# Optimization experiments

Hardware: AMD Instinct MI355X
Metric: run time of the kernel (lower is better)

The kernel has to match this reference:

```python
import jax, jax.numpy as jnp
import numpy as np

N = 50000      # nodes
E = 800000     # edges (before self-loops)
H = 4          # heads
NEG_SLOPE = 0.2
EPS = 1e-16


def setup_inputs() -> dict:
    key = jax.random.key(0)
    ks = jax.random.split(key, 10)
    m, hidden, m_y = 128, 32, 32
    x = jax.random.normal(ks[0], (N, m), jnp.float32)
    edge_index = jax.random.randint(ks[1], (2, E), 0, N, jnp.int32)
    s1 = 1.0 / np.sqrt(m)
    s2 = 1.0 / np.sqrt(H * hidden)
    W1 = jax.random.normal(ks[2], (m, H * hidden), jnp.float32) * s1
    a1_src = jax.random.normal(ks[3], (H, hidden), jnp.float32) * s1
    a1_dst = jax.random.normal(ks[4], (H, hidden), jnp.float32) * s1
    b1 = jnp.zeros((H * hidden,), jnp.float32)
    W2 = jax.random.normal(ks[5], (H * hidden, H * m_y), jnp.float32) * s2
    a2_src = jax.random.normal(ks[6], (H, m_y), jnp.float32) * s2
    a2_dst = jax.random.normal(ks[7], (H, m_y), jnp.float32) * s2
    b2 = jnp.zeros((H * m_y,), jnp.float32)
    return {"x": x, "edge_index": edge_index, "W1": W1, "a1_src": a1_src,
            "a1_dst": a1_dst, "b1": b1, "W2": W2, "a2_src": a2_src,
            "a2_dst": a2_dst, "b2": b2}


def gat_conv(x, W, a_src, a_dst, bias, src, dst):
    # x: [N, F_in], W: [F_in, H*C]
    C = a_src.shape[1]
    h = (x @ W).reshape(N, H, C)                      # [N, H, C]
    alpha_s = jnp.einsum('nhc,hc->nh', h, a_src)       # [N, H]
    alpha_d = jnp.einsum('nhc,hc->nh', h, a_dst)       # [N, H]
    e = jax.nn.leaky_relu(alpha_s[src] + alpha_d[dst], NEG_SLOPE)  # [Etot, H]
    # segment softmax over incoming edges of each dst node
    e_max = jax.ops.segment_max(e, dst, num_segments=N)            # [N, H]
    e_exp = jnp.exp(e - e_max[dst])
    denom = jax.ops.segment_sum(e_exp, dst, num_segments=N)        # [N, H]
    alpha = e_exp / (denom[dst] + EPS)                             # [Etot, H]
    out = jax.ops.segment_sum(h[src] * alpha[:, :, None], dst, num_segments=N)
    return out.reshape(N, H * C) + bias


def reference(x, edge_index, W1, a1_src, a1_dst, b1, W2, a2_src, a2_dst, b2):
    # add self-loops (PyG GATConv default add_self_loops=True)
    loops = jnp.arange(N, dtype=edge_index.dtype)
    src = jnp.concatenate([edge_index[0], loops])
    dst = jnp.concatenate([edge_index[1], loops])
    out = gat_conv(x, W1, a1_src, a1_dst, b1, src, dst)
    out = jax.nn.elu(out)
    # dropout(p=0.8) is identity in eval mode
    out = gat_conv(out, W2, a2_src, a2_dst, b2, src, dst)
    return out
```

## Files before the change

kernel.cpp:

```cpp
#include <hip/hip_runtime.h>
#include <math.h>
#include <stdint.h>

typedef __attribute__((ext_vector_type(8))) short short8;
typedef __attribute__((ext_vector_type(4))) float f32x4;

static __device__ __forceinline__ float lrelu(float x) { return x >= 0.f ? x : 0.2f * x; }

static __device__ __forceinline__ uint32_t f2bf(float f) {
    uint32_t u = __float_as_uint(f);
    return (u + 0x7FFFu + ((u >> 16) & 1u)) >> 16;
}

__global__ __launch_bounds__(256) void count_wprep(const int* __restrict__ dst, int E, int N,
                                                   int* __restrict__ deg8,
                                                   int* __restrict__ rank, int eb,
                                                   const float* __restrict__ W1,
                                                   const float* __restrict__ W2,
                                                   uint16_t* __restrict__ wtb1,
                                                   uint16_t* __restrict__ wtb2) {
    if ((int)blockIdx.x < eb) {
        int i = blockIdx.x * 256 + threadIdx.x;
        int p = blockIdx.x & 7;
        if (i < E) rank[i] = atomicAdd(&deg8[p * N + dst[i]], 1);
    } else {
        int idx = (blockIdx.x - eb) * 256 + threadIdx.x;
        const float* src = (idx < 16384) ? W1 : W2;
        uint16_t* dw = (idx < 16384) ? wtb1 : wtb2;
        int j = idx & 16383;
        dw[(j & 127) * 128 + (j >> 7)] = (uint16_t)f2bf(src[j]);
    }
}

__global__ __launch_bounds__(256) void scan1(const int* __restrict__ deg8, int N, int ntot,
                                             int* __restrict__ deg,
                                             int* __restrict__ base8,
                                             int* __restrict__ rowptr,
                                             int* __restrict__ csum) {
    __shared__ int s[256];
    int t = threadIdx.x;
    int i = blockIdx.x * 256 + t;
    int v = 0;
    if (i < N) {
        int total = 0;
        #pragma unroll
        for (int p = 0; p < 8; ++p) {
            int c = deg8[p * N + i];
            base8[p * N + i] = total;
            total += c;
        }
        deg[i] = total;
        v = (total + 15) & ~15;
    }
    s[t] = v;
    __syncthreads();
    #pragma unroll
    for (int off = 1; off < 256; off <<= 1) {
        int add = (t >= off) ? s[t - off] : 0;
        __syncthreads();
        s[t] += add;
        __syncthreads();
    }
    if (i < ntot) rowptr[i] = s[t] - v;
    if (t == 255) csum[blockIdx.x] = s[255];
}

__global__ __launch_bounds__(256) void scan2(const int* __restrict__ csum,
                                             int* __restrict__ coff, int nch) {
    __shared__ int s[256];
    int t = threadIdx.x;
    int v = (t < nch) ? csum[t] : 0;
    s[t] = v;
    __syncthreads();
    #pragma unroll
    for (int off = 1; off < 256; off <<= 1) {
        int add = (t >= off) ? s[t - off] : 0;
        __syncthreads();
        s[t] += add;
        __syncthreads();
    }
    coff[t] = s[t] - v;
}

__global__ __launch_bounds__(256) void scan3(int* __restrict__ rowptr,
                                             const int* __restrict__ coff, int ntot) {
    int i = blockIdx.x * 256 + threadIdx.x;
    if (i < ntot) rowptr[i] += coff[blockIdx.x];
}

__global__ __launch_bounds__(256) void fill_pad(const int* __restrict__ src,
                                                const int* __restrict__ dst,
                                                const int* __restrict__ rank, int E, int N,
                                                const int* __restrict__ rowptr,
                                                const int* __restrict__ deg,
                                                const int* __restrict__ base8,
                                                uint16_t* __restrict__ colidx,
                                                float* __restrict__ as_,
                                                uint32_t* __restrict__ hbf, int eb) {
    if ((int)blockIdx.x < eb) {
        int i = blockIdx.x * 256 + threadIdx.x;
        int p = blockIdx.x & 7;
        if (i < E) {
            int d = dst[i];
            colidx[rowptr[d] + base8[p * N + d] + rank[i]] = (uint16_t)src[i];
        }
    } else {
        int i = (blockIdx.x - eb) * 256 + threadIdx.x;
        if (i < 4) as_[N * 4 + i] = -1e30f;
        if (i < 64) hbf[(size_t)N * 64 + i] = 0u;
        if (i < N) {
            int b = rowptr[i] + deg[i];
            int e = rowptr[i + 1];
            for (int pp = b; pp < e; ++pp) colidx[pp] = (uint16_t)N;
        }
    }
}

__global__ __launch_bounds__(256) void gemm_mfma(const float* __restrict__ x,
                                                 const uint16_t* __restrict__ wtb,
                                                 const float* __restrict__ a_src,
                                                 const float* __restrict__ a_dst,
                                                 uint32_t* __restrict__ hbf,
                                                 float* __restrict__ as_,
                                                 float* __restrict__ ad_,
                                                 int nrows) {
    __shared__ __align__(16) char lds[52224];
    const int t = threadIdx.x;
    const int row0 = blockIdx.x * 64;

    {
        int r = t >> 2;
        int k16b = (t & 3) * 4;
        const float* xrow = x + (size_t)(row0 + r) * 128;
        bool ok = (row0 + r) < nrows;
        #pragma unroll
        for (int i = 0; i < 4; ++i) {
            int k16 = k16b + i;
            float4 va = make_float4(0.f, 0.f, 0.f, 0.f), vb = va;
            if (ok) {
                va = *(const float4*)(xrow + k16 * 8);
                vb = *(const float4*)(xrow + k16 * 8 + 4);
            }
            uint4 pk;
            pk.x = f2bf(va.x) | (f2bf(va.y) << 16);
            pk.y = f2bf(va.z) | (f2bf(va.w) << 16);
            pk.z = f2bf(vb.x) | (f2bf(vb.y) << 16);
            pk.w = f2bf(vb.z) | (f2bf(vb.w) << 16);
            *(uint4*)(lds + r * 272 + k16 * 16) = pk;
        }
    }
    {
        #pragma unroll
        for (int i = 0; i < 8; ++i) {
            int u = t * 8 + i;
            int col = u >> 4, k16 = u & 15;
            uint4 v = *(const uint4*)(wtb + col * 128 + k16 * 8);
            *(uint4*)(lds + 17408 + col * 272 + k16 * 16) = v;
        }
    }
    __syncthreads();

    const int w = t >> 6, lane = t & 63;
    const int wrow0 = w * 16;
    const int la = lane & 15, lb = lane >> 4;

    f32x4 acc[8];
    #pragma unroll
    for (int ct = 0; ct < 8; ++ct) acc[ct] = (f32x4){0.f, 0.f, 0.f, 0.f};

    const char* xsb = lds + (wrow0 + la) * 272;
    const char* wsb = lds + 17408;
    #pragma unroll
    for (int kc = 0; kc < 4; ++kc) {
        int k16 = kc * 4 + lb;
        short8 a = *(const short8*)(xsb + k16 * 16);
        #pragma unroll
        for (int ct = 0; ct < 8; ++ct) {
            int col = ct * 16 + la;
            short8 b = *(const short8*)(wsb + col * 272 + k16 * 16);
            acc[ct] = __builtin_amdgcn_mfma_f32_16x16x32_bf16(a, b, acc[ct], 0, 0, 0);
        }
    }
    __syncthreads();

    float* scr = (float*)lds;
    #pragma unroll
    for (int ct = 0; ct < 8; ++ct)
        #pragma unroll
        for (int r2 = 0; r2 < 4; ++r2)
            scr[(wrow0 + lb * 4 + r2) * 132 + ct * 16 + la] = acc[ct][r2];
    __syncthreads();

    {
        int row = t >> 2, q = t & 3;
        int grow = row0 + row;
        float v[32];
        #pragma unroll
        for (int m = 0; m < 8; ++m) {
            float4 f = *(const float4*)(scr + row * 132 + q * 32 + m * 4);
            v[m * 4 + 0] = f.x; v[m * 4 + 1] = f.y;
            v[m * 4 + 2] = f.z; v[m * 4 + 3] = f.w;
        }
        if (grow < nrows) {
            uint32_t* orow = hbf + (size_t)grow * 64 + q * 16;
            #pragma unroll
            for (int m2 = 0; m2 < 4; ++m2) {
                uint4 pk;
                pk.x = f2bf(v[m2 * 8 + 0]) | (f2bf(v[m2 * 8 + 1]) << 16);
                pk.y = f2bf(v[m2 * 8 + 2]) | (f2bf(v[m2 * 8 + 3]) << 16);
                pk.z = f2bf(v[m2 * 8 + 4]) | (f2bf(v[m2 * 8 + 5]) << 16);
                pk.w = f2bf(v[m2 * 8 + 6]) | (f2bf(v[m2 * 8 + 7]) << 16);
                *(uint4*)(orow + m2 * 4) = pk;
            }
            float ps = 0.f, pd = 0.f;
            const float* asp = a_src + q * 32;
            const float* adp = a_dst + q * 32;
            #pragma unroll
            for (int j = 0; j < 32; ++j) {
                ps = fmaf(v[j], asp[j], ps);
                pd = fmaf(v[j], adp[j], pd);
            }
            as_[grow * 4 + q] = ps;
            ad_[grow * 4 + q] = pd;
        }
    }
}

__global__ __launch_bounds__(256) void aggregate(const uint32_t* __restrict__ hb,
                                                 const float* __restrict__ as_,
                                                 const float* __restrict__ ad_,
                                                 const int* __restrict__ rowptr,
                                                 const uint16_t* __restrict__ colidx,
                                                 const float* __restrict__ bias,
                                                 float* __restrict__ out, int n, int do_elu) {
    int node = blockIdx.x * 4 + (threadIdx.x >> 6);
    if (node >= n) return;
    int lane = threadIdx.x & 63;
    int hd = lane >> 4;
    int k = lane * 2;
    int ce = lane >> 2;
    int ch = lane & 3;
    float adn = ad_[node * 4 + hd];
    float adc = ad_[node * 4 + ch];
    float accx = 0.f, accy = 0.f, denom = 0.f;

    {
        float wgt = __expf(lrelu(as_[node * 4 + hd] + adn));
        uint32_t u = hb[(size_t)node * 64 + lane];
        accx = fmaf(wgt, __uint_as_float(u << 16), accx);
        accy = fmaf(wgt, __uint_as_float(u & 0xFFFF0000u), accy);
        denom += wgt;
    }
    const int beg = rowptr[node], end = rowptr[node + 1];
    for (int j = beg; j < end; j += 16) {
        uint4 cA = *(const uint4*)(colidx + j);
        uint4 cB = *(const uint4*)(colidx + j + 8);
        int sE[16];
        sE[0]  = cA.x & 0xFFFF; sE[1]  = cA.x >> 16;
        sE[2]  = cA.y & 0xFFFF; sE[3]  = cA.y >> 16;
        sE[4]  = cA.z & 0xFFFF; sE[5]  = cA.z >> 16;
        sE[6]  = cA.w & 0xFFFF; sE[7]  = cA.w >> 16;
        sE[8]  = cB.x & 0xFFFF; sE[9]  = cB.x >> 16;
        sE[10] = cB.y & 0xFFFF; sE[11] = cB.y >> 16;
        sE[12] = cB.z & 0xFFFF; sE[13] = cB.z >> 16;
        sE[14] = cB.w & 0xFFFF; sE[15] = cB.w >> 16;
        int sw = colidx[j + ce];
        float aw = as_[sw * 4 + ch];
        uint32_t u[16];
        #pragma unroll
        for (int e = 0; e < 16; ++e) u[e] = hb[(size_t)sE[e] * 64 + lane];
        float w = __expf(lrelu(aw + adc));
        #pragma unroll
        for (int e = 0; e < 16; ++e) {
            float we = __shfl(w, e * 4 + hd);
            accx = fmaf(we, __uint_as_float(u[e] << 16), accx);
            accy = fmaf(we, __uint_as_float(u[e] & 0xFFFF0000u), accy);
            denom += we;
        }
    }
    float inv = 1.f / (denom + 1e-16f);
    float o0 = fmaf(accx, inv, bias[k]);
    float o1 = fmaf(accy, inv, bias[k + 1]);
    if (do_elu) {
        o0 = o0 > 0.f ? o0 : (__expf(o0) - 1.f);
        o1 = o1 > 0.f ? o1 : (__expf(o1) - 1.f);
    }
    *(float2*)&out[(size_t)node * 128 + k] = make_float2(o0, o1);
}

extern "C" void kernel_launch(void* const* d_in, const int* in_sizes, int n_in,
                              void* d_out, int out_size, void* d_ws, size_t ws_size,
                              hipStream_t stream) {
    const float* x   = (const float*)d_in[0];
    const int*   ei  = (const int*)d_in[1];
    const float* W1  = (const float*)d_in[2];
    const float* a1s = (const float*)d_in[3];
    const float* a1d = (const float*)d_in[4];
    const float* b1  = (const float*)d_in[5];
    const float* W2  = (const float*)d_in[6];
    const float* a2s = (const float*)d_in[7];
    const float* a2d = (const float*)d_in[8];
    const float* b2  = (const float*)d_in[9];
    float* out = (float*)d_out;

    const int N = in_sizes[0] / 128;
    const int E = in_sizes[1] / 2;
    const int* esrc = ei;
    const int* edst = ei + E;

    char* w = (char*)d_ws;
    uint32_t* hbf  = (uint32_t*)w; w += (size_t)(N + 1) * 64 * 4;
    float*    as_  = (float*)w;    w += (size_t)(N + 1) * 4 * 4;
    float*    ad_  = (float*)w;    w += (size_t)(N + 1) * 4 * 4;
    int* deg    = (int*)w;   w += (size_t)N * 4;
    int* rowptr = (int*)w;   w += (size_t)(N + 1) * 4;
    int* rank   = (int*)w;   w += (size_t)E * 4;
    int* deg8   = (int*)w;   w += (size_t)8 * N * 4;
    int* base8  = (int*)w;   w += (size_t)8 * N * 4;
    int* csum   = (int*)w;   w += 256 * 4;
    int* coff   = (int*)w;   w += 256 * 4;
    uint16_t* wtb1 = (uint16_t*)w; w += 16384 * 2;
    uint16_t* wtb2 = (uint16_t*)w; w += 16384 * 2;
    w = (char*)(((uintptr_t)w + 31) & ~(uintptr_t)31);
    uint16_t* colidx = (uint16_t*)w; w += ((size_t)E + 16ull * N) * 2;
    float* out1 = out;

    hipMemsetAsync(deg8, 0, (size_t)8 * N * 4, stream);

    const int eb = (E + 255) / 256;
    const int ntot = N + 1;
    const int nch = (ntot + 255) / 256;
    const int gb = (N + 63) / 64;
    const int nb = (N + 3) / 4;
    const int pb = (N + 255) / 256;

    count_wprep<<<eb + 128, 256, 0, stream>>>(edst, E, N, deg8, rank, eb,
                                              W1, W2, wtb1, wtb2);
    scan1<<<nch, 256, 0, stream>>>(deg8, N, ntot, deg, base8, rowptr, csum);
    scan2<<<1, 256, 0, stream>>>(csum, coff, nch);
    scan3<<<nch, 256, 0, stream>>>(rowptr, coff, ntot);
    fill_pad<<<eb + pb, 256, 0, stream>>>(esrc, edst, rank, E, N, rowptr, deg,
                                          base8, colidx, as_, hbf, eb);

    gemm_mfma<<<gb, 256, 0, stream>>>(x, wtb1, a1s, a1d, hbf, as_, ad_, N);
    aggregate<<<nb, 256, 0, stream>>>(hbf, as_, ad_, rowptr, colidx, b1, out1, N, 1);

    gemm_mfma<<<gb, 256, 0, stream>>>(out1, wtb2, a2s, a2d, hbf, as_, ad_, N);
    aggregate<<<nb, 256, 0, stream>>>(hbf, as_, ad_, rowptr, colidx, b2, out, N, 0);
}
```

Before: 261.7 us.

## Split aggregate wavefront into four edge groups using 16-byte row gathers

Reorganizes the per-node aggregation so each wavefront splits into four 16-lane groups. Each group gathers a full 256-byte bf16 feature row with uint4 loads, and the four groups work on different edges at the same time. Partial sums are combined with cross-group shuffles and the self-loop term is added at the end. This replaces sixteen 4-byte per-lane gathers per chunk with four 16-byte gathers and fewer shuffles, aiming to raise memory-level efficiency. The cost is more accumulator registers, a final reduction, and only a quarter of the lanes doing the store.

New measurement: 265.2 us. Within noise of the previous version (+1.3%).

```diff
diff --git a/kernel.cpp b/kernel.cpp
--- a/kernel.cpp
+++ b/kernel.cpp
@@ -11,6 +11,8 @@
     uint32_t u = __float_as_uint(f);
     return (u + 0x7FFFu + ((u >> 16) & 1u)) >> 16;
 }
+static __device__ __forceinline__ float bflo(uint32_t u) { return __uint_as_float(u << 16); }
+static __device__ __forceinline__ float bfhi(uint32_t u) { return __uint_as_float(u & 0xFFFF0000u); }
 
 __global__ __launch_bounds__(256) void count_wprep(const int* __restrict__ dst, int E, int N,
                                                    int* __restrict__ deg8,
@@ -235,57 +237,94 @@
                                                  float* __restrict__ out, int n, int do_elu) {
     int node = blockIdx.x * 4 + (threadIdx.x >> 6);
     if (node >= n) return;
-    int lane = threadIdx.x & 63;
-    int hd = lane >> 4;
-    int k = lane * 2;
-    int ce = lane >> 2;
-    int ch = lane & 3;
+    int L = threadIdx.x & 63;
+    int g16 = L & 15;
+    int grp = L >> 4;
+    int hd = g16 >> 2;
+    int cw_e = L >> 2;
+    int cw_h = L & 3;
     float adn = ad_[node * 4 + hd];
-    float adc = ad_[node * 4 + ch];
-    float accx = 0.f, accy = 0.f, denom = 0.f;
-
-    {
-        float wgt = __expf(lrelu(as_[node * 4 + hd] + adn));
-        uint32_t u = hb[(size_t)node * 64 + lane];
-        accx = fmaf(wgt, __uint_as_float(u << 16), accx);
-        accy = fmaf(wgt, __uint_as_float(u & 0xFFFF0000u), accy);
-        denom += wgt;
-    }
+    float adc = ad_[node * 4 + cw_h];
+
+    float acc[8];
+    #pragma unroll
+    for (int i = 0; i < 8; ++i) acc[i] = 0.f;
+    float den = 0.f;
+
     const int beg = rowptr[node], end = rowptr[node + 1];
     for (int j = beg; j < end; j += 16) {
-        uint4 cA = *(const uint4*)(colidx + j);
-        uint4 cB = *(const uint4*)(colidx + j + 8);
-        int sE[16];
-        sE[0]  = cA.x & 0xFFFF; sE[1]  = cA.x >> 16;
-        sE[2]  = cA.y & 0xFFFF; sE[3]  = cA.y >> 16;
-        sE[4]  = cA.z & 0xFFFF; sE[5]  = cA.z >> 16;
-        sE[6]  = cA.w & 0xFFFF; sE[7]  = cA.w >> 16;
-        sE[8]  = cB.x & 0xFFFF; sE[9]  = cB.x >> 16;
-        sE[10] = cB.y & 0xFFFF; sE[11] = cB.y >> 16;
-        sE[12] = cB.z & 0xFFFF; sE[13] = cB.z >> 16;
-        sE[14] = cB.w & 0xFFFF; sE[15] = cB.w >> 16;
-        int sw = colidx[j + ce];
-        float aw = as_[sw * 4 + ch];
-        uint32_t u[16];
-        #pragma unroll
-        for (int e = 0; e < 16; ++e) u[e] = hb[(size_t)sE[e] * 64 + lane];
-        float w = __expf(lrelu(aw + adc));
-        #pragma unroll
-        for (int e = 0; e < 16; ++e) {
-            float we = __shfl(w, e * 4 + hd);
-            accx = fmaf(we, __uint_as_float(u[e] << 16), accx);
-            accy = fmaf(we, __uint_as_float(u[e] & 0xFFFF0000u), accy);
-            denom += we;
-        }
-    }
-    float inv = 1.f / (denom + 1e-16f);
-    float o0 = fmaf(accx, inv, bias[k]);
-    float o1 = fmaf(accy, inv, bias[k + 1]);
-    if (do_elu) {
-        o0 = o0 > 0.f ? o0 : (__expf(o0) - 1.f);
-        o1 = o1 > 0.f ? o1 : (__expf(o1) - 1.f);
-    }
-    *(float2*)&out[(size_t)node * 128 + k] = make_float2(o0, o1);
+        int sw = colidx[j + cw_e];
+        float w = __expf(lrelu(as_[sw * 4 + cw_h] + adc));
+        uint4 u0, u1, u2, u3;
+        {
+            int s0 = colidx[j + grp];
+            int s1 = colidx[j + 4 + grp];
+            int s2 = colidx[j + 8 + grp];
+            int s3 = colidx[j + 12 + grp];
+            u0 = *(const uint4*)(hb + (size_t)s0 * 64 + g16 * 4);
+            u1 = *(const uint4*)(hb + (size_t)s1 * 64 + g16 * 4);
+            u2 = *(const uint4*)(hb + (size_t)s2 * 64 + g16 * 4);
+            u3 = *(const uint4*)(hb + (size_t)s3 * 64 + g16 * 4);
+        }
+        float w0 = __shfl(w, ((0 * 4 + grp) << 2) | hd);
+        float w1 = __shfl(w, ((1 * 4 + grp) << 2) | hd);
+        float w2 = __shfl(w, ((2 * 4 + grp) << 2) | hd);
+        float w3 = __shfl(w, ((3 * 4 + grp) << 2) | hd);
+        acc[0] = fmaf(w0, bflo(u0.x), acc[0]); acc[1] = fmaf(w0, bfhi(u0.x), acc[1]);
+        acc[2] = fmaf(w0, bflo(u0.y), acc[2]); acc[3] = fmaf(w0, bfhi(u0.y), acc[3]);
+        acc[4] = fmaf(w0, bflo(u0.z), acc[4]); acc[5] = fmaf(w0, bfhi(u0.z), acc[5]);
+        acc[6] = fmaf(w0, bflo(u0.w), acc[6]); acc[7] = fmaf(w0, bfhi(u0.w), acc[7]);
+        acc[0] = fmaf(w1, bflo(u1.x), acc[0]); acc[1] = fmaf(w1, bfhi(u1.x), acc[1]);
+        acc[2] = fmaf(w1, bflo(u1.y), acc[2]); acc[3] = fmaf(w1, bfhi(u1.y), acc[3]);
+        acc[4] = fmaf(w1, bflo(u1.z), acc[4]); acc[5] = fmaf(w1, bfhi(u1.z), acc[5]);
+        acc[6] = fmaf(w1, bflo(u1.w), acc[6]); acc[7] = fmaf(w1, bfhi(u1.w), acc[7]);
+        acc[0] = fmaf(w2, bflo(u2.x), acc[0]); acc[1] = fmaf(w2, bfhi(u2.x), acc[1]);
+        acc[2] = fmaf(w2, bflo(u2.y), acc[2]); acc[3] = fmaf(w2, bfhi(u2.y), acc[3]);
+        acc[4] = fmaf(w2, bflo(u2.z), acc[4]); acc[5] = fmaf(w2, bfhi(u2.z), acc[5]);
+        acc[6] = fmaf(w2, bflo(u2.w), acc[6]); acc[7] = fmaf(w2, bfhi(u2.w), acc[7]);
+        acc[0] = fmaf(w3, bflo(u3.x), acc[0]); acc[1] = fmaf(w3, bfhi(u3.x), acc[1]);
+        acc[2] = fmaf(w3, bflo(u3.y), acc[2]); acc[3] = fmaf(w3, bfhi(u3.y), acc[3]);
+        acc[4] = fmaf(w3, bflo(u3.z), acc[4]); acc[5] = fmaf(w3, bfhi(u3.z), acc[5]);
+        acc[6] = fmaf(w3, bflo(u3.w), acc[6]); acc[7] = fmaf(w3, bfhi(u3.w), acc[7]);
+        den += (w0 + w1) + (w2 + w3);
+    }
+
+    #pragma unroll
+    for (int i = 0; i < 8; ++i) {
+        acc[i] += __shfl_xor(acc[i], 16);
+        acc[i] += __shfl_xor(acc[i], 32);
+    }
+    den += __shfl_xor(den, 16);
+    den += __shfl_xor(den, 32);
+
+    {
+        float ws = __expf(lrelu(as_[node * 4 + hd] + adn));
+        uint4 us = *(const uint4*)(hb + (size_t)node * 64 + g16 * 4);
+        acc[0] = fmaf(ws, bflo(us.x), acc[0]); acc[1] = fmaf(ws, bfhi(us.x), acc[1]);
+        acc[2] = fmaf(ws, bflo(us.y), acc[2]); acc[3] = fmaf(ws, bfhi(us.y), acc[3]);
+        acc[4] = fmaf(ws, bflo(us.z), acc[4]); acc[5] = fmaf(ws, bfhi(us.z), acc[5]);
+        acc[6] = fmaf(ws, bflo(us.w), acc[6]); acc[7] = fmaf(ws, bfhi(us.w), acc[7]);
+        den += ws;
+    }
+
+    if (grp == 0) {
+        float inv = 1.f / (den + 1e-16f);
+        float4 b0 = *(const float4*)(bias + g16 * 8);
+        float4 b1 = *(const float4*)(bias + g16 * 8 + 4);
+        float o[8];
+        o[0] = fmaf(acc[0], inv, b0.x); o[1] = fmaf(acc[1], inv, b0.y);
+        o[2] = fmaf(acc[2], inv, b0.z); o[3] = fmaf(acc[3], inv, b0.w);
+        o[4] = fmaf(acc[4], inv, b1.x); o[5] = fmaf(acc[5], inv, b1.y);
+        o[6] = fmaf(acc[6], inv, b1.z); o[7] = fmaf(acc[7], inv, b1.w);
+        if (do_elu) {
+            #pragma unroll
+            for (int i = 0; i < 8; ++i)
+                o[i] = o[i] > 0.f ? o[i] : (__expf(o[i]) - 1.f);
+        }
+        float* orow = out + (size_t)node * 128 + g16 * 8;
+        *(float4*)orow       = make_float4(o[0], o[1], o[2], o[3]);
+        *(float4*)(orow + 4) = make_float4(o[4], o[5], o[6], o[7]);
+    }
 }
 
 extern "C" void kernel_launch(void* const* d_in, const int* in_sizes, int n_in,
```

## Split features into eight column slices and aggregate each slice separately

Applied to the files above, without the earlier changes.

The bf16 node-feature table is stored as eight column slices (16 features each, 32 bytes per node) instead of one 256-byte row per node. Aggregation launches 8x the blocks, one per slice, so each slice table is smaller and more likely to stay in cache during random gathers; within a wave, lanes split edges into groups and reduce by shuffle. The self-loop now sits in the padded CSR (one extra slot per row) instead of being a special case. In exchange, attention weights are recomputed eight times per edge and each wave does less useful work per gather.

Result: slower. 484.3 us (+85.1%).

```diff
diff --git a/kernel.cpp b/kernel.cpp
--- a/kernel.cpp
+++ b/kernel.cpp
@@ -11,6 +11,8 @@
     uint32_t u = __float_as_uint(f);
     return (u + 0x7FFFu + ((u >> 16) & 1u)) >> 16;
 }
+static __device__ __forceinline__ float bflo(uint32_t u) { return __uint_as_float(u << 16); }
+static __device__ __forceinline__ float bfhi(uint32_t u) { return __uint_as_float(u & 0xFFFF0000u); }
 
 __global__ __launch_bounds__(256) void count_wprep(const int* __restrict__ dst, int E, int N,
                                                    int* __restrict__ deg8,
@@ -50,7 +52,7 @@
             total += c;
         }
         deg[i] = total;
-        v = (total + 15) & ~15;
+        v = (total + 16) & ~15;
     }
     s[t] = v;
     __syncthreads();
@@ -96,7 +98,8 @@
                                                 const int* __restrict__ base8,
                                                 uint16_t* __restrict__ colidx,
                                                 float* __restrict__ as_,
-                                                uint32_t* __restrict__ hbf, int eb) {
+                                                uint32_t* __restrict__ hbh, int eb) {
+    int N1 = N + 1;
     if ((int)blockIdx.x < eb) {
         int i = blockIdx.x * 256 + threadIdx.x;
         int p = blockIdx.x & 7;
@@ -107,11 +110,12 @@
     } else {
         int i = (blockIdx.x - eb) * 256 + threadIdx.x;
         if (i < 4) as_[N * 4 + i] = -1e30f;
-        if (i < 64) hbf[(size_t)N * 64 + i] = 0u;
+        if (i < 64) hbh[(size_t)(i >> 3) * (N1 * 8) + (size_t)N * 8 + (i & 7)] = 0u;
         if (i < N) {
             int b = rowptr[i] + deg[i];
             int e = rowptr[i + 1];
-            for (int pp = b; pp < e; ++pp) colidx[pp] = (uint16_t)N;
+            colidx[b] = (uint16_t)i;
+            for (int pp = b + 1; pp < e; ++pp) colidx[pp] = (uint16_t)N;
         }
     }
 }
@@ -120,10 +124,10 @@
                                                  const uint16_t* __restrict__ wtb,
                                                  const float* __restrict__ a_src,
                                                  const float* __restrict__ a_dst,
-                                                 uint32_t* __restrict__ hbf,
+                                                 uint32_t* __restrict__ hbh,
                                                  float* __restrict__ as_,
                                                  float* __restrict__ ad_,
-                                                 int nrows) {
+                                                 int nrows, int N1) {
     __shared__ __align__(16) char lds[52224];
     const int t = threadIdx.x;
     const int row0 = blockIdx.x * 64;
@@ -202,16 +206,18 @@
             v[m * 4 + 2] = f.z; v[m * 4 + 3] = f.w;
         }
         if (grow < nrows) {
-            uint32_t* orow = hbf + (size_t)grow * 64 + q * 16;
+            uint4 pk[4];
             #pragma unroll
             for (int m2 = 0; m2 < 4; ++m2) {
-                uint4 pk;
-                pk.x = f2bf(v[m2 * 8 + 0]) | (f2bf(v[m2 * 8 + 1]) << 16);
-                pk.y = f2bf(v[m2 * 8 + 2]) | (f2bf(v[m2 * 8 + 3]) << 16);
-                pk.z = f2bf(v[m2 * 8 + 4]) | (f2bf(v[m2 * 8 + 5]) << 16);
-                pk.w = f2bf(v[m2 * 8 + 6]) | (f2bf(v[m2 * 8 + 7]) << 16);
-                *(uint4*)(orow + m2 * 4) = pk;
+                pk[m2].x = f2bf(v[m2 * 8 + 0]) | (f2bf(v[m2 * 8 + 1]) << 16);
+                pk[m2].y = f2bf(v[m2 * 8 + 2]) | (f2bf(v[m2 * 8 + 3]) << 16);
+                pk[m2].z = f2bf(v[m2 * 8 + 4]) | (f2bf(v[m2 * 8 + 5]) << 16);
+                pk[m2].w = f2bf(v[m2 * 8 + 6]) | (f2bf(v[m2 * 8 + 7]) << 16);
             }
+            uint32_t* r0 = hbh + (size_t)(2 * q) * (N1 * 8) + (size_t)grow * 8;
+            uint32_t* r1 = hbh + (size_t)(2 * q + 1) * (N1 * 8) + (size_t)grow * 8;
+            *(uint4*)r0 = pk[0]; *(uint4*)(r0 + 4) = pk[1];
+            *(uint4*)r1 = pk[2]; *(uint4*)(r1 + 4) = pk[3];
             float ps = 0.f, pd = 0.f;
             const float* asp = a_src + q * 32;
             const float* adp = a_dst + q * 32;
@@ -226,66 +232,53 @@
     }
 }
 
-__global__ __launch_bounds__(256) void aggregate(const uint32_t* __restrict__ hb,
+__global__ __launch_bounds__(256) void aggregate(const uint32_t* __restrict__ hbh,
                                                  const float* __restrict__ as_,
                                                  const float* __restrict__ ad_,
                                                  const int* __restrict__ rowptr,
                                                  const uint16_t* __restrict__ colidx,
                                                  const float* __restrict__ bias,
-                                                 float* __restrict__ out, int n, int do_elu) {
-    int node = blockIdx.x * 4 + (threadIdx.x >> 6);
+                                                 float* __restrict__ out,
+                                                 int n, int N1, int do_elu) {
+    int b = blockIdx.x;
+    int s = b & 7;
+    int node = (b >> 3) * 4 + (threadIdx.x >> 6);
     if (node >= n) return;
-    int lane = threadIdx.x & 63;
-    int hd = lane >> 4;
-    int k = lane * 2;
-    int ce = lane >> 2;
-    int ch = lane & 3;
-    float adn = ad_[node * 4 + hd];
-    float adc = ad_[node * 4 + ch];
-    float accx = 0.f, accy = 0.f, denom = 0.f;
-
-    {
-        float wgt = __expf(lrelu(as_[node * 4 + hd] + adn));
-        uint32_t u = hb[(size_t)node * 64 + lane];
-        accx = fmaf(wgt, __uint_as_float(u << 16), accx);
-        accy = fmaf(wgt, __uint_as_float(u & 0xFFFF0000u), accy);
-        denom += wgt;
-    }
+    int h = s >> 1;
+    int L = threadIdx.x & 63;
+    int d = L & 7;
+    int g = L >> 3;
+    const uint32_t* hb = hbh + (size_t)s * (N1 * 8);
+    float adn = ad_[node * 4 + h];
+    float ax = 0.f, ay = 0.f, den = 0.f;
+
     const int beg = rowptr[node], end = rowptr[node + 1];
     for (int j = beg; j < end; j += 16) {
-        uint4 cA = *(const uint4*)(colidx + j);
-        uint4 cB = *(const uint4*)(colidx + j + 8);
-        int sE[16];
-        sE[0]  = cA.x & 0xFFFF; sE[1]  = cA.x >> 16;
-        sE[2]  = cA.y & 0xFFFF; sE[3]  = cA.y >> 16;
-        sE[4]  = cA.z & 0xFFFF; sE[5]  = cA.z >> 16;
-        sE[6]  = cA.w & 0xFFFF; sE[7]  = cA.w >> 16;
-        sE[8]  = cB.x & 0xFFFF; sE[9]  = cB.x >> 16;
-        sE[10] = cB.y & 0xFFFF; sE[11] = cB.y >> 16;
-        sE[12] = cB.z & 0xFFFF; sE[13] = cB.z >> 16;
-        sE[14] = cB.w & 0xFFFF; sE[15] = cB.w >> 16;
-        int sw = colidx[j + ce];
-        float aw = as_[sw * 4 + ch];
-        uint32_t u[16];
-        #pragma unroll
-        for (int e = 0; e < 16; ++e) u[e] = hb[(size_t)sE[e] * 64 + lane];
-        float w = __expf(lrelu(aw + adc));
-        #pragma unroll
-        for (int e = 0; e < 16; ++e) {
-            float we = __shfl(w, e * 4 + hd);
-            accx = fmaf(we, __uint_as_float(u[e] << 16), accx);
-            accy = fmaf(we, __uint_as_float(u[e] & 0xFFFF0000u), accy);
-            denom += we;
-        }
-    }
-    float inv = 1.f / (denom + 1e-16f);
-    float o0 = fmaf(accx, inv, bias[k]);
-    float o1 = fmaf(accy, inv, bias[k + 1]);
-    if (do_elu) {
-        o0 = o0 > 0.f ? o0 : (__expf(o0) - 1.f);
-        o1 = o1 > 0.f ? o1 : (__expf(o1) - 1.f);
-    }
-    *(float2*)&out[(size_t)node * 128 + k] = make_float2(o0, o1);
+        int ce = __builtin_nontemporal_load(&colidx[j + (L & 15)]);
+        float w = __expf(lrelu(as_[ce * 4 + h] + adn));
+        int s0 = __shfl(ce, g), s1 = __shfl(ce, 8 + g);
+        float w0 = __shfl(w, g), w1 = __shfl(w, 8 + g);
+        uint32_t u0 = hb[(size_t)s0 * 8 + d];
+        uint32_t u1 = hb[(size_t)s1 * 8 + d];
+        ax = fmaf(w0, bflo(u0), ax); ay = fmaf(w0, bfhi(u0), ay);
+        ax = fmaf(w1, bflo(u1), ax); ay = fmaf(w1, bfhi(u1), ay);
+        den += w0 + w1;
+    }
+    ax += __shfl_xor(ax, 8);  ax += __shfl_xor(ax, 16);  ax += __shfl_xor(ax, 32);
+    ay += __shfl_xor(ay, 8);  ay += __shfl_xor(ay, 16);  ay += __shfl_xor(ay, 32);
+    den += __shfl_xor(den, 8); den += __shfl_xor(den, 16); den += __shfl_xor(den, 32);
+
+    if (L < 8) {
+        float inv = 1.f / (den + 1e-16f);
+        int c = s * 16 + d * 2;
+        float o0 = fmaf(ax, inv, bias[c]);
+        float o1 = fmaf(ay, inv, bias[c + 1]);
+        if (do_elu) {
+            o0 = o0 > 0.f ? o0 : (__expf(o0) - 1.f);
+            o1 = o1 > 0.f ? o1 : (__expf(o1) - 1.f);
+        }
+        *(float2*)&out[(size_t)node * 128 + c] = make_float2(o0, o1);
+    }
 }
 
 extern "C" void kernel_launch(void* const* d_in, const int* in_sizes, int n_in,
@@ -305,15 +298,16 @@
 
     const int N = in_sizes[0] / 128;
     const int E = in_sizes[1] / 2;
+    const int N1 = N + 1;
     const int* esrc = ei;
     const int* edst = ei + E;
 
     char* w = (char*)d_ws;
-    uint32_t* hbf  = (uint32_t*)w; w += (size_t)(N + 1) * 64 * 4;
-    float*    as_  = (float*)w;    w += (size_t)(N + 1) * 4 * 4;
-    float*    ad_  = (float*)w;    w += (size_t)(N + 1) * 4 * 4;
+    uint32_t* hbh  = (uint32_t*)w; w += (size_t)N1 * 64 * 4;
+    float*    as_  = (float*)w;    w += (size_t)N1 * 4 * 4;
+    float*    ad_  = (float*)w;    w += (size_t)N1 * 4 * 4;
     int* deg    = (int*)w;   w += (size_t)N * 4;
-    int* rowptr = (int*)w;   w += (size_t)(N + 1) * 4;
+    int* rowptr = (int*)w;   w += (size_t)N1 * 4;
     int* rank   = (int*)w;   w += (size_t)E * 4;
     int* deg8   = (int*)w;   w += (size_t)8 * N * 4;
     int* base8  = (int*)w;   w += (size_t)8 * N * 4;
@@ -322,7 +316,7 @@
     uint16_t* wtb1 = (uint16_t*)w; w += 16384 * 2;
     uint16_t* wtb2 = (uint16_t*)w; w += 16384 * 2;
     w = (char*)(((uintptr_t)w + 31) & ~(uintptr_t)31);
-    uint16_t* colidx = (uint16_t*)w; w += ((size_t)E + 16ull * N) * 2;
+    uint16_t* colidx = (uint16_t*)w; w += ((size_t)E + 16ull * N + 16) * 2;
     float* out1 = out;
 
     hipMemsetAsync(deg8, 0, (size_t)8 * N * 4, stream);
@@ -331,7 +325,7 @@
     const int ntot = N + 1;
     const int nch = (ntot + 255) / 256;
     const int gb = (N + 63) / 64;
-    const int nb = (N + 3) / 4;
+    const int nb2 = 8 * ((N + 3) / 4);
     const int pb = (N + 255) / 256;
 
     count_wprep<<<eb + 128, 256, 0, stream>>>(edst, E, N, deg8, rank, eb,
@@ -340,11 +334,11 @@
     scan2<<<1, 256, 0, stream>>>(csum, coff, nch);
     scan3<<<nch, 256, 0, stream>>>(rowptr, coff, ntot);
     fill_pad<<<eb + pb, 256, 0, stream>>>(esrc, edst, rank, E, N, rowptr, deg,
-                                          base8, colidx, as_, hbf, eb);
-
-    gemm_mfma<<<gb, 256, 0, stream>>>(x, wtb1, a1s, a1d, hbf, as_, ad_, N);
-    aggregate<<<nb, 256, 0, stream>>>(hbf, as_, ad_, rowptr, colidx, b1, out1, N, 1);
-
-    gemm_mfma<<<gb, 256, 0, stream>>>(out1, wtb2, a2s, a2d, hbf, as_, ad_, N);
-    aggregate<<<nb, 256, 0, stream>>>(hbf, as_, ad_, rowptr, colidx, b2, out, N, 0);
-}
+                                          base8, colidx, as_, hbh, eb);
+
+    gemm_mfma<<<gb, 256, 0, stream>>>(x, wtb1, a1s, a1d, hbh, as_, ad_, N, N1);
+    aggregate<<<nb2, 256, 0, stream>>>(hbh, as_, ad_, rowptr, colidx, b1, out1, N, N1, 1);
+
+    gemm_mfma<<<gb, 256, 0, stream>>>(out1, wtb2, a2s, a2d, hbh, as_, ad_, N, N1);
+    aggregate<<<nb2, 256, 0, stream>>>(hbh, as_, ad_, rowptr, colidx, b2, out, N, N1, 0);
+}
```
